# Optimization experiments

Measured on AMD Instinct MI355X. Metric: run time of the kernel, lower is better.

The kernel has to match this reference:

```python
import jax, jax.numpy as jnp
import numpy as np

N_PRED = 29
F_DIM = 8192
H1 = 256
H2 = 128


def setup_inputs() -> dict:
    key = jax.random.key(0)
    ks = jax.random.split(key, 7)
    features = jax.random.normal(ks[0], (4096, F_DIM), dtype=jnp.float32)
    # Stacked per-predicate MLP weights (PyTorch Linear init scale ~ 1/sqrt(fan_in))
    W1 = jax.random.normal(ks[1], (N_PRED, F_DIM, H1), dtype=jnp.float32) / np.sqrt(F_DIM)
    b1 = jax.random.normal(ks[2], (N_PRED, H1), dtype=jnp.float32) / np.sqrt(F_DIM)
    W2 = jax.random.normal(ks[3], (N_PRED, H1, H2), dtype=jnp.float32) / np.sqrt(H1)
    b2 = jax.random.normal(ks[4], (N_PRED, H2), dtype=jnp.float32) / np.sqrt(H1)
    W3 = jax.random.normal(ks[5], (N_PRED, H2), dtype=jnp.float32) / np.sqrt(H2)
    b3 = jax.random.normal(ks[6], (N_PRED,), dtype=jnp.float32) / np.sqrt(H2)
    return {"features": features, "W1": W1, "b1": b1, "W2": W2, "b2": b2, "W3": W3, "b3": b3}


def reference(features, W1, b1, W2, b2, W3, b3):
    # 29 parallel heads as one batched (grouped) GEMM chain; dropout = identity (eval).
    h1 = jax.nn.relu(jnp.einsum('bf,pfh->bph', features, W1) + b1[None])   # [B, P, H1]
    h2 = jax.nn.relu(jnp.einsum('bph,phk->bpk', h1, W2) + b2[None])        # [B, P, H2]
    logits = jnp.einsum('bpk,pk->bp', h2, W3) + b3[None]                   # [B, P]
    return jax.nn.sigmoid(logits)
```

## Files before the change

kernel.cpp:

```cpp
#include <hip/hip_runtime.h>
#include <hip/hip_bf16.h>

typedef __attribute__((ext_vector_type(8))) short short8_t;
typedef __attribute__((ext_vector_type(8))) __bf16 bf16x8;
typedef __attribute__((ext_vector_type(4))) float f32x4;

__device__ __forceinline__ void gload16(const void* g, void* l) {
  __builtin_amdgcn_global_load_lds(
      (const __attribute__((address_space(1))) void*)g,
      (__attribute__((address_space(3))) void*)l, 16, 0, 0);
}

__device__ __forceinline__ unsigned short f2bf(float f) {
  __hip_bfloat16 h = __float2bfloat16(f);
  return __builtin_bit_cast(unsigned short, h);
}

#define BARRIER() asm volatile("s_barrier" ::: "memory")


__global__ void k_cvt_feat(const float* __restrict__ in, unsigned short* __restrict__ out) {
  const size_t N = (size_t)4096 * 8192;
  size_t i = ((size_t)blockIdx.x * 256 + threadIdx.x) * 4;
  const size_t stride = (size_t)gridDim.x * 256 * 4;
  for (; i < N; i += stride) {
    float4 v = *(const float4*)(in + i);
    ushort4 o;
    o.x = f2bf(v.x); o.y = f2bf(v.y); o.z = f2bf(v.z); o.w = f2bf(v.w);
    *(ushort4*)(out + i) = o;
  }
}

__global__ void k_cvt_w1(const float* __restrict__ W1, unsigned short* __restrict__ out, int p0) {
  __shared__ unsigned short t[64][66];
  const int p = p0 + blockIdx.z;
  const float* src = W1 + (size_t)p * 8192 * 256;
  unsigned short* dst = out + (size_t)blockIdx.z * 256 * 8192;
  const int f0 = blockIdx.x * 64, h0 = blockIdx.y * 64;
#pragma unroll
  for (int i = 0; i < 16; ++i) {
    int tt = i * 256 + threadIdx.x;
    int r = tt >> 6, c = tt & 63;
    t[r][c] = f2bf(src[(size_t)(f0 + r) * 256 + h0 + c]);
  }
  __syncthreads();
#pragma unroll
  for (int i = 0; i < 16; ++i) {
    int tt = i * 256 + threadIdx.x;
    int r = tt >> 6, c = tt & 63;
    dst[(size_t)(h0 + r) * 8192 + f0 + c] = t[c][r];
  }
}

__global__ void k_cvt_w2(const float* __restrict__ W2, unsigned short* __restrict__ out) {
  const int p = blockIdx.x;
  const float* src = W2 + (size_t)p * 256 * 128;
  unsigned short* dst = out + (size_t)p * 128 * 256;
  for (int tt = threadIdx.x; tt < 128 * 256; tt += 256) {
    int j = tt >> 8, h = tt & 255;
    dst[tt] = f2bf(src[(size_t)h * 128 + j]);
  }
}

__global__ __launch_bounds__(512, 2) void k_gemm1(
    const unsigned short* __restrict__ A,
    const unsigned short* __restrict__ Bt,
    const float* __restrict__ b1,
    unsigned short* __restrict__ h1,
    int p0) {
  __shared__ __align__(16) unsigned short S[65536];

  const int tid = threadIdx.x;
  const int lane = tid & 63;
  const int wave = tid >> 6;
  const int sr = (wave >> 2) * 64;
  const int sc = (wave & 3) * 32;

  const int nz = gridDim.y;
  const int nwg = gridDim.x * nz;
  const int orig = blockIdx.y * gridDim.x + blockIdx.x;
  const int q = nwg >> 3, r_ = nwg & 7;
  const int xcd = orig & 7, idx = orig >> 3;
  const int wg = (xcd < r_ ? xcd * (q + 1) : r_ * (q + 1) + (xcd - r_) * q) + idx;
  const int mx = wg / nz;
  const int z = wg % nz;
  const int p = p0 + z;
  const int m0 = mx * 256;

  const unsigned short* Ab = A + (size_t)m0 * 8192;
  const unsigned short* Bb = Bt + (size_t)z * 256 * 8192;

  int e0 = tid, r0 = e0 >> 3, u0 = (e0 & 7) ^ (r0 & 7);
  int e1 = 512 + tid, r1e = e1 >> 3, u1 = (e1 & 7) ^ (r1e & 7);
  const size_t s0 = (size_t)r0 * 8192 + u0 * 8;
  const size_t s1 = (size_t)r1e * 8192 + u1 * 8;
  const int ld0 = (wave * 64) * 8;
  const int ld1 = (512 + wave * 64) * 8;

  auto stage = [&](int buf, int isB, int h, int T) {
    const unsigned short* gb = (isB ? Bb : Ab) + (size_t)h * 128 * 8192 + (size_t)T * 64;
    unsigned short* lb = S + buf * 32768 + isB * 16384 + h * 8192;
    gload16(gb + s0, lb + ld0);
    gload16(gb + s1, lb + ld1);
  };

  const int l15 = lane & 15, ks = lane >> 4;

  auto rdA = [&](int buf, int h, int mi, int x) {
    int R = sr + mi * 16 + l15;
    int pu = (x * 4 + ks) ^ (R & 7);
    return __builtin_bit_cast(bf16x8, *(const short8_t*)(S + buf * 32768 + h * 8192 + R * 64 + pu * 8));
  };
  auto rdB = [&](int buf, int v, int nj, int x) {
    int R = sc + nj * 16 + l15;
    int pu = (x * 4 + ks) ^ (R & 7);
    return __builtin_bit_cast(bf16x8, *(const short8_t*)(S + buf * 32768 + 16384 + v * 8192 + R * 64 + pu * 8));
  };

  f32x4 acc[4][4][2] = {};
  const int NT = 8192 / 64;

  auto kstep = [&](int t, int pf, int vm1, int vm4) {
    const int c = t & 1, nx = c ^ 1;
    bf16x8 a[4][2], bl[2][2], bh[2][2];
#pragma unroll
    for (int mi = 0; mi < 4; ++mi) { a[mi][0] = rdA(c, 0, mi, 0); a[mi][1] = rdA(c, 0, mi, 1); }
#pragma unroll
    for (int nj = 0; nj < 2; ++nj) { bl[nj][0] = rdB(c, 0, nj, 0); bl[nj][1] = rdB(c, 0, nj, 1); }
    if (pf) { stage(nx, 0, 0, t + 1); stage(nx, 1, 0, t + 1); }
    BARRIER();
    __builtin_amdgcn_s_setprio(1);
#pragma unroll
    for (int mi = 0; mi < 4; ++mi)
#pragma unroll
      for (int nj = 0; nj < 2; ++nj) {
        acc[0][mi][nj] = __builtin_amdgcn_mfma_f32_16x16x32_bf16(a[mi][0], bl[nj][0], acc[0][mi][nj], 0, 0, 0);
        acc[0][mi][nj] = __builtin_amdgcn_mfma_f32_16x16x32_bf16(a[mi][1], bl[nj][1], acc[0][mi][nj], 0, 0, 0);
      }
    __builtin_amdgcn_s_setprio(0);
    if (vm1 == 4)      asm volatile("s_waitcnt vmcnt(4)" ::: "memory");
    else if (vm1 == 0) asm volatile("s_waitcnt vmcnt(0)" ::: "memory");
    BARRIER();
#pragma unroll
    for (int nj = 0; nj < 2; ++nj) { bh[nj][0] = rdB(c, 1, nj, 0); bh[nj][1] = rdB(c, 1, nj, 1); }
    BARRIER();
    __builtin_amdgcn_s_setprio(1);
#pragma unroll
    for (int mi = 0; mi < 4; ++mi)
#pragma unroll
      for (int nj = 0; nj < 2; ++nj) {
        acc[1][mi][nj] = __builtin_amdgcn_mfma_f32_16x16x32_bf16(a[mi][0], bh[nj][0], acc[1][mi][nj], 0, 0, 0);
        acc[1][mi][nj] = __builtin_amdgcn_mfma_f32_16x16x32_bf16(a[mi][1], bh[nj][1], acc[1][mi][nj], 0, 0, 0);
      }
    __builtin_amdgcn_s_setprio(0);
    BARRIER();
#pragma unroll
    for (int mi = 0; mi < 4; ++mi) { a[mi][0] = rdA(c, 1, mi, 0); a[mi][1] = rdA(c, 1, mi, 1); }
    if (pf) { stage(nx, 1, 1, t + 1); stage(nx, 0, 1, t + 1); }
    BARRIER();
    __builtin_amdgcn_s_setprio(1);
#pragma unroll
    for (int mi = 0; mi < 4; ++mi)
#pragma unroll
      for (int nj = 0; nj < 2; ++nj) {
        acc[2][mi][nj] = __builtin_amdgcn_mfma_f32_16x16x32_bf16(a[mi][0], bl[nj][0], acc[2][mi][nj], 0, 0, 0);
        acc[2][mi][nj] = __builtin_amdgcn_mfma_f32_16x16x32_bf16(a[mi][1], bl[nj][1], acc[2][mi][nj], 0, 0, 0);
      }
    __builtin_amdgcn_s_setprio(0);
    BARRIER();
    __builtin_amdgcn_s_setprio(1);
#pragma unroll
    for (int mi = 0; mi < 4; ++mi)
#pragma unroll
      for (int nj = 0; nj < 2; ++nj) {
        acc[3][mi][nj] = __builtin_amdgcn_mfma_f32_16x16x32_bf16(a[mi][0], bh[nj][0], acc[3][mi][nj], 0, 0, 0);
        acc[3][mi][nj] = __builtin_amdgcn_mfma_f32_16x16x32_bf16(a[mi][1], bh[nj][1], acc[3][mi][nj], 0, 0, 0);
      }
    __builtin_amdgcn_s_setprio(0);
    if (vm4 == 4)      asm volatile("s_waitcnt vmcnt(4)" ::: "memory");
    else if (vm4 == 0) asm volatile("s_waitcnt vmcnt(0)" ::: "memory");
    BARRIER();
  };

  stage(0, 0, 0, 0); stage(0, 1, 0, 0);
  stage(0, 1, 1, 0); stage(0, 0, 1, 0);
  asm volatile("s_waitcnt vmcnt(4)" ::: "memory");
  BARRIER();

  for (int t = 0; t < NT - 1; ++t) kstep(t, 1, 4, 4);
  kstep(NT - 1, 0, 0, -1);

  const int rg = lane >> 4;
#pragma unroll
  for (int qh = 0; qh < 2; ++qh)
#pragma unroll
    for (int qv = 0; qv < 2; ++qv) {
      const int qq = qh * 2 + qv;
#pragma unroll
      for (int nj = 0; nj < 2; ++nj) {
        const int col = qv * 128 + sc + nj * 16 + l15;
        const float bb = b1[p * 256 + col];
#pragma unroll
        for (int mi = 0; mi < 4; ++mi) {
          const int rbase = m0 + qh * 128 + sr + mi * 16 + rg * 4;
#pragma unroll
          for (int rr = 0; rr < 4; ++rr) {
            float v = acc[qq][mi][nj][rr] + bb;
            v = v > 0.f ? v : 0.f;
            h1[((size_t)p * 4096 + rbase + rr) * 256 + col] = f2bf(v);
          }
        }
      }
    }
}

__global__ __launch_bounds__(256, 2) void k_gemm23(
    const unsigned short* __restrict__ h1,
    const unsigned short* __restrict__ W2t,
    const float* __restrict__ b2,
    const float* __restrict__ W3,
    const float* __restrict__ b3,
    float* __restrict__ out) {
  __shared__ __align__(16) unsigned short lds_a[128 * 64];
  __shared__ __align__(16) unsigned short lds_b[128 * 64];
  const int tid = threadIdx.x;
  const int lane = tid & 63;
  const int wave = tid >> 6;
  const int m0 = blockIdx.x * 128;
  const int p = blockIdx.y;

  const unsigned short* Ab = h1 + ((size_t)p * 4096 + m0) * 256;
  const unsigned short* Bb = W2t + (size_t)p * 128 * 256;

  f32x4 acc[2][8] = {};

  for (int k0 = 0; k0 < 256; k0 += 64) {
    __syncthreads();
#pragma unroll
    for (int i = 0; i < 4; ++i) {
      int t = i * 256 + tid;
      int r = t >> 3;
      int uu = (t & 7) ^ (r & 7);
      gload16(Ab + (size_t)r * 256 + k0 + uu * 8, &lds_a[(i * 256 + wave * 64) * 8]);
      gload16(Bb + (size_t)r * 256 + k0 + uu * 8, &lds_b[(i * 256 + wave * 64) * 8]);
    }
    __syncthreads();
#pragma unroll
    for (int kk = 0; kk < 64; kk += 32) {
      const int ku = (kk >> 3) + (lane >> 4);
      bf16x8 af[2], bfv[8];
#pragma unroll
      for (int mi = 0; mi < 2; ++mi) {
        int row = wave * 32 + mi * 16 + (lane & 15);
        int u = ku ^ (row & 7);
        af[mi] = __builtin_bit_cast(bf16x8, *(const short8_t*)&lds_a[row * 64 + u * 8]);
      }
#pragma unroll
      for (int nj = 0; nj < 8; ++nj) {
        int row = nj * 16 + (lane & 15);
        int u = ku ^ (row & 7);
        bfv[nj] = __builtin_bit_cast(bf16x8, *(const short8_t*)&lds_b[row * 64 + u * 8]);
      }
#pragma unroll
      for (int mi = 0; mi < 2; ++mi)
#pragma unroll
        for (int nj = 0; nj < 8; ++nj)
          acc[mi][nj] = __builtin_amdgcn_mfma_f32_16x16x32_bf16(af[mi], bfv[nj], acc[mi][nj], 0, 0, 0);
    }
  }

  float b2v[8], w3v[8];
  const int c16 = lane & 15;
#pragma unroll
  for (int nj = 0; nj < 8; ++nj) {
    int c = nj * 16 + c16;
    b2v[nj] = b2[p * 128 + c];
    w3v[nj] = W3[p * 128 + c];
  }
  const float b3p = b3[p];
#pragma unroll
  for (int mi = 0; mi < 2; ++mi) {
#pragma unroll
    for (int r = 0; r < 4; ++r) {
      float s = 0.f;
#pragma unroll
      for (int nj = 0; nj < 8; ++nj) {
        float v = acc[mi][nj][r] + b2v[nj];
        v = v > 0.f ? v : 0.f;
        s += v * w3v[nj];
      }
      s += __shfl_xor(s, 1);
      s += __shfl_xor(s, 2);
      s += __shfl_xor(s, 4);
      s += __shfl_xor(s, 8);
      if ((lane & 15) == 0) {
        int m = m0 + wave * 32 + mi * 16 + (lane >> 4) * 4 + r;
        float logit = s + b3p;
        out[(size_t)m * 29 + p] = 1.f / (1.f + __expf(-logit));
      }
    }
  }
}

extern "C" void kernel_launch(void* const* d_in, const int* in_sizes, int n_in,
                              void* d_out, int out_size, void* d_ws, size_t ws_size,
                              hipStream_t stream) {
  const float* features = (const float*)d_in[0];
  const float* W1 = (const float*)d_in[1];
  const float* b1 = (const float*)d_in[2];
  const float* W2 = (const float*)d_in[3];
  const float* b2 = (const float*)d_in[4];
  const float* W3 = (const float*)d_in[5];
  const float* b3 = (const float*)d_in[6];
  float* out = (float*)d_out;

  char* ws = (char*)d_ws;
  const size_t featB = (size_t)4096 * 8192 * 2;
  const size_t h1B   = (size_t)29 * 4096 * 256 * 2;
  const size_t w2B   = (size_t)29 * 128 * 256 * 2;
  const size_t w1pp  = (size_t)256 * 8192 * 2;

  unsigned short* featbf = (unsigned short*)ws;
  unsigned short* h1bf   = (unsigned short*)(ws + featB);
  unsigned short* w2t    = (unsigned short*)(ws + featB + h1B);
  unsigned short* w1t    = (unsigned short*)(ws + featB + h1B + w2B);

  size_t base = featB + h1B + w2B;
  size_t rem = (ws_size > base) ? (ws_size - base) : 0;
  int CH = (int)(rem / w1pp);
  if (CH > 29) CH = 29;
  if (CH < 1) CH = 1;

  k_cvt_feat<<<2048, 256, 0, stream>>>(features, featbf);
  k_cvt_w2<<<29, 256, 0, stream>>>(W2, w2t);

  for (int p0 = 0; p0 < 29; p0 += CH) {
    int c = (29 - p0) < CH ? (29 - p0) : CH;
    k_cvt_w1<<<dim3(128, 4, c), 256, 0, stream>>>(W1, w1t, p0);
    k_gemm1<<<dim3(16, c), 512, 0, stream>>>(featbf, w1t, b1, h1bf, p0);
  }

  k_gemm23<<<dim3(32, 29), 256, 0, stream>>>(h1bf, w2t, b2, W3, b3, out);
}
```

Before: 563.2 us.

## Deepen GEMM1 prefetch to two k-tiles ahead and remap workgroup order

```diff
diff --git a/kernel.cpp b/kernel.cpp
--- a/kernel.cpp
+++ b/kernel.cpp
@@ -76,14 +76,13 @@
   const int sr = (wave >> 2) * 64;
   const int sc = (wave & 3) * 32;
 
-  const int nz = gridDim.y;
-  const int nwg = gridDim.x * nz;
+  const int nwg = gridDim.x * gridDim.y;
   const int orig = blockIdx.y * gridDim.x + blockIdx.x;
   const int q = nwg >> 3, r_ = nwg & 7;
   const int xcd = orig & 7, idx = orig >> 3;
   const int wg = (xcd < r_ ? xcd * (q + 1) : r_ * (q + 1) + (xcd - r_) * q) + idx;
-  const int mx = wg / nz;
-  const int z = wg % nz;
+  const int mx = wg & 15;
+  const int z = wg >> 4;
   const int p = p0 + z;
   const int m0 = mx * 256;
 
@@ -120,14 +119,13 @@
   f32x4 acc[4][4][2] = {};
   const int NT = 8192 / 64;
 
-  auto kstep = [&](int t, int pf, int vm1, int vm4) {
-    const int c = t & 1, nx = c ^ 1;
+  auto kstep = [&](int t, int pf, int vm) {
+    const int c = t & 1;
     bf16x8 a[4][2], bl[2][2], bh[2][2];
 #pragma unroll
     for (int mi = 0; mi < 4; ++mi) { a[mi][0] = rdA(c, 0, mi, 0); a[mi][1] = rdA(c, 0, mi, 1); }
 #pragma unroll
     for (int nj = 0; nj < 2; ++nj) { bl[nj][0] = rdB(c, 0, nj, 0); bl[nj][1] = rdB(c, 0, nj, 1); }
-    if (pf) { stage(nx, 0, 0, t + 1); stage(nx, 1, 0, t + 1); }
     BARRIER();
     __builtin_amdgcn_s_setprio(1);
 #pragma unroll
@@ -138,11 +136,10 @@
         acc[0][mi][nj] = __builtin_amdgcn_mfma_f32_16x16x32_bf16(a[mi][1], bl[nj][1], acc[0][mi][nj], 0, 0, 0);
       }
     __builtin_amdgcn_s_setprio(0);
-    if (vm1 == 4)      asm volatile("s_waitcnt vmcnt(4)" ::: "memory");
-    else if (vm1 == 0) asm volatile("s_waitcnt vmcnt(0)" ::: "memory");
     BARRIER();
 #pragma unroll
     for (int nj = 0; nj < 2; ++nj) { bh[nj][0] = rdB(c, 1, nj, 0); bh[nj][1] = rdB(c, 1, nj, 1); }
+    if (pf) stage(c, 0, 0, t + 2);
     BARRIER();
     __builtin_amdgcn_s_setprio(1);
 #pragma unroll
@@ -156,7 +153,7 @@
     BARRIER();
 #pragma unroll
     for (int mi = 0; mi < 4; ++mi) { a[mi][0] = rdA(c, 1, mi, 0); a[mi][1] = rdA(c, 1, mi, 1); }
-    if (pf) { stage(nx, 1, 1, t + 1); stage(nx, 0, 1, t + 1); }
+    if (pf) stage(c, 1, 1, t + 2);
     BARRIER();
     __builtin_amdgcn_s_setprio(1);
 #pragma unroll
@@ -168,6 +165,7 @@
       }
     __builtin_amdgcn_s_setprio(0);
     BARRIER();
+    if (pf) { stage(c, 1, 0, t + 2); stage(c, 0, 1, t + 2); }
     __builtin_amdgcn_s_setprio(1);
 #pragma unroll
     for (int mi = 0; mi < 4; ++mi)
@@ -177,18 +175,19 @@
         acc[3][mi][nj] = __builtin_amdgcn_mfma_f32_16x16x32_bf16(a[mi][1], bh[nj][1], acc[3][mi][nj], 0, 0, 0);
       }
     __builtin_amdgcn_s_setprio(0);
-    if (vm4 == 4)      asm volatile("s_waitcnt vmcnt(4)" ::: "memory");
-    else if (vm4 == 0) asm volatile("s_waitcnt vmcnt(0)" ::: "memory");
+    if (vm == 8)      asm volatile("s_waitcnt vmcnt(8)" ::: "memory");
+    else if (vm == 0) asm volatile("s_waitcnt vmcnt(0)" ::: "memory");
     BARRIER();
   };
 
-  stage(0, 0, 0, 0); stage(0, 1, 0, 0);
-  stage(0, 1, 1, 0); stage(0, 0, 1, 0);
-  asm volatile("s_waitcnt vmcnt(4)" ::: "memory");
+  stage(0, 0, 0, 0); stage(0, 1, 0, 0); stage(0, 1, 1, 0); stage(0, 0, 1, 0);
+  stage(1, 0, 0, 1); stage(1, 1, 1, 1); stage(1, 1, 0, 1); stage(1, 0, 1, 1);
+  asm volatile("s_waitcnt vmcnt(8)" ::: "memory");
   BARRIER();
 
-  for (int t = 0; t < NT - 1; ++t) kstep(t, 1, 4, 4);
-  kstep(NT - 1, 0, 0, -1);
+  for (int t = 0; t < NT - 2; ++t) kstep(t, 1, 8);
+  kstep(NT - 2, 0, 0);
+  kstep(NT - 1, 0, -1);
 
   const int rg = lane >> 4;
 #pragma unroll
```

Measured after the change: 548.3 us. 2.6% less time.
